# Kernel tuning notes

Hardware: AMD Instinct MI355X
Metric: run time of the kernel (lower is better)

Reference implementation:

```python
import jax, jax.numpy as jnp
import numpy as np

N_EMBD = 1024
N_HEAD = 16
HEAD_SIZE = 64


def setup_inputs() -> dict:
    key = jax.random.key(0)
    ks = jax.random.split(key, 6)
    B, T, C, H, D = 2, 2048, N_EMBD, N_HEAD, HEAD_SIZE
    s = 1.0 / np.sqrt(C)
    x = jax.random.normal(ks[0], (B, T, C), dtype=jnp.float32)
    Wq = jax.random.normal(ks[1], (H, C, D), dtype=jnp.float32) * s
    Wk = jax.random.normal(ks[2], (H, C, D), dtype=jnp.float32) * s
    Wv = jax.random.normal(ks[3], (H, C, D), dtype=jnp.float32) * s
    Wo = jax.random.normal(ks[4], (H * D, C), dtype=jnp.float32) * (1.0 / np.sqrt(H * D))
    bo = jax.random.normal(ks[5], (C,), dtype=jnp.float32) * 0.01
    return {"x": x, "Wq": Wq, "Wk": Wk, "Wv": Wv, "Wo": Wo, "bo": bo}


def reference(x, Wq, Wk, Wv, Wo, bo):
    B, T, C = x.shape
    H, _, D = Wq.shape
    # Per-head projections, batched across heads: [B,H,T,D]
    q = jnp.einsum('btc,hcd->bhtd', x, Wq)
    k = jnp.einsum('btc,hcd->bhtd', x, Wk)
    v = jnp.einsum('btc,hcd->bhtd', x, Wv)
    # NOTE: original scales by sqrt(C) = sqrt(n_embd), not sqrt(head_size)
    scale = 1.0 / jnp.sqrt(jnp.float32(C))
    att = jnp.einsum('bhtd,bhsd->bhts', q, k) * scale  # [B,H,T,T]
    causal = jnp.tril(jnp.ones((T, T), dtype=bool))
    att = jnp.where(causal, att, -jnp.inf)
    att = jax.nn.softmax(att, axis=-1)
    # dropout omitted (eval mode / deterministic reference)
    out = jnp.einsum('bhts,bhsd->bhtd', att, v)  # [B,H,T,D]
    out = out.transpose(0, 2, 1, 3).reshape(B, T, H * D)
    return out @ Wo + bo
```

## Files before the change

### kernel.cpp

```cpp
#include <hip/hip_runtime.h>
#include <hip/hip_bf16.h>


typedef __hip_bfloat16 bf16;
typedef __bf16 v8bf __attribute__((ext_vector_type(8)));
typedef float  v4f  __attribute__((ext_vector_type(4)));
typedef unsigned long long u64;
typedef unsigned int u32;

#define MFMA16(a, b, c) __builtin_amdgcn_mfma_f32_16x16x32_bf16((a), (b), (c), 0, 0, 0)

__device__ __forceinline__ bf16 f2b(float x) { return __float2bfloat16(x); }
__device__ __forceinline__ __bf16 f2braw(float x) {
  bf16 t = __float2bfloat16(x);
  return *reinterpret_cast<__bf16*>(&t);
}
__device__ __forceinline__ unsigned short f2bu(float x) {
  bf16 t = __float2bfloat16(x);
  return *reinterpret_cast<unsigned short*>(&t);
}

__device__ __forceinline__ void load16_lds(const bf16* gptr, const bf16* lptr) {
  __builtin_amdgcn_global_load_lds(
      (const __attribute__((address_space(1))) u32*)gptr,
      (__attribute__((address_space(3))) u32*)lptr, 16, 0, 0);
}

__global__ __launch_bounds__(256) void prep_kernel(
    const float* __restrict__ x,
    const float* __restrict__ Wq, const float* __restrict__ Wk,
    const float* __restrict__ Wv, const float* __restrict__ Wo,
    bf16* __restrict__ xb, bf16* __restrict__ wt, bf16* __restrict__ wot)
{
  __shared__ float Lt[32][33];
  const int bid = blockIdx.x, tid = threadIdx.x;

  if (bid < 2048) {
    size_t i = ((size_t)bid * 256 + tid) * 8;
    float4 f0 = *(const float4*)(x + i);
    float4 f1 = *(const float4*)(x + i + 4);
    v8bf v;
    v[0] = f2braw(f0.x); v[1] = f2braw(f0.y); v[2] = f2braw(f0.z); v[3] = f2braw(f0.w);
    v[4] = f2braw(f1.x); v[5] = f2braw(f1.y); v[6] = f2braw(f1.z); v[7] = f2braw(f1.w);
    *(v8bf*)(xb + i) = v;
    return;
  }
  const int tx = tid & 31, ty = tid >> 5;
  if (bid < 5120) {
    const int idx = bid - 2048;
    const int z = idx >> 6, rem = idx & 63;
    const int p = z >> 4, h = z & 15;
    const float* ib = ((p == 0) ? Wq : (p == 1) ? Wk : Wv) + (size_t)h * 65536;
    bf16* ob = wt + (size_t)z * 65536;
    const int j0 = (rem & 1) * 32, i0 = (rem >> 1) * 32;
    #pragma unroll
    for (int r = 0; r < 4; ++r)
      Lt[ty + 8 * r][tx] = ib[(size_t)(i0 + ty + 8 * r) * 64 + j0 + tx];
    __syncthreads();
    #pragma unroll
    for (int r = 0; r < 4; ++r)
      ob[(size_t)(j0 + ty + 8 * r) * 1024 + i0 + tx] = f2b(Lt[tx][ty + 8 * r]);
  } else {
    const int idx = bid - 5120;
    const int j0 = (idx & 31) * 32, i0 = (idx >> 5) * 32;
    #pragma unroll
    for (int r = 0; r < 4; ++r)
      Lt[ty + 8 * r][tx] = Wo[(size_t)(i0 + ty + 8 * r) * 1024 + j0 + tx];
    __syncthreads();
    #pragma unroll
    for (int r = 0; r < 4; ++r)
      wot[(size_t)(j0 + ty + 8 * r) * 1024 + i0 + tx] = f2b(Lt[tx][ty + 8 * r]);
  }
}

__global__ __launch_bounds__(256) void qkv_gemm_kernel(
    const bf16* __restrict__ xb, const bf16* __restrict__ wt,
    bf16* __restrict__ qkv)
{
  __shared__ __align__(16) bf16 Ash[2][128][32];
  __shared__ __align__(16) bf16 Bsh[2][128][32];

  const int mt = blockIdx.x, nt = blockIdx.y;
  const int tid = threadIdx.x, w = tid >> 6, lane = tid & 63;
  const int ln = lane & 15, quad = lane >> 4;
  const int wm = w >> 1, wn = w & 1;
  const int m0 = mt * 128, n0 = nt * 128;

  const v4f vzero = {0.f, 0.f, 0.f, 0.f};
  v4f acc[4][4];
  #pragma unroll
  for (int mf = 0; mf < 4; ++mf)
    #pragma unroll
    for (int nf = 0; nf < 4; ++nf) acc[mf][nf] = vzero;

  const int srow = lane >> 2, sseg = (lane & 3) * 8;
  const bf16* ga = xb + (size_t)(m0 + 32 * w + srow) * 1024 + sseg;
  const bf16* gb = wt + (size_t)(n0 + 32 * w + srow) * 1024 + sseg;

  {
    load16_lds(ga,             &Ash[0][32 * w][0]);
    load16_lds(ga + 16 * 1024, &Ash[0][32 * w + 16][0]);
    load16_lds(gb,             &Bsh[0][32 * w][0]);
    load16_lds(gb + 16 * 1024, &Bsh[0][32 * w + 16][0]);
  }

  for (int kt = 0; kt < 32; ++kt) {
    const int buf = kt & 1;
    __syncthreads();

    v8bf af[4], bfv[4];
    #pragma unroll
    for (int mf = 0; mf < 4; ++mf)
      af[mf] = *(const v8bf*)&Ash[buf][wm * 64 + mf * 16 + ln][quad * 8];
    #pragma unroll
    for (int nf = 0; nf < 4; ++nf)
      bfv[nf] = *(const v8bf*)&Bsh[buf][wn * 64 + nf * 16 + ln][quad * 8];

    if (kt < 31) {
      const int k0 = (kt + 1) * 32, nb = buf ^ 1;
      load16_lds(ga + k0,             &Ash[nb][32 * w][0]);
      load16_lds(ga + 16 * 1024 + k0, &Ash[nb][32 * w + 16][0]);
      load16_lds(gb + k0,             &Bsh[nb][32 * w][0]);
      load16_lds(gb + 16 * 1024 + k0, &Bsh[nb][32 * w + 16][0]);
    }

    #pragma unroll
    for (int mf = 0; mf < 4; ++mf)
      #pragma unroll
      for (int nf = 0; nf < 4; ++nf)
        acc[mf][nf] = MFMA16(af[mf], bfv[nf], acc[mf][nf]);
  }

  const int jcol0 = n0 + wn * 64;
  const int p = jcol0 >> 10;
  const int h = (jcol0 >> 6) & 15;
  const float scale = (p == 0) ? 0.03125f : 1.0f;

  if (p < 2) {
    bf16* base = qkv + (size_t)p * 4194304 + (size_t)h * 262144;
    #pragma unroll
    for (int mf = 0; mf < 4; ++mf)
      #pragma unroll
      for (int nf = 0; nf < 4; ++nf) {
        int d = nf * 16 + ln;
        #pragma unroll
        for (int r = 0; r < 4; ++r) {
          int m = m0 + wm * 64 + mf * 16 + quad * 4 + r;
          base[(size_t)m * 64 + d] = f2b(acc[mf][nf][r] * scale);
        }
      }
  } else {
    bf16* vb = qkv + (size_t)2 * 4194304 + (size_t)h * 262144;
    #pragma unroll
    for (int mf = 0; mf < 4; ++mf) {
      int mrow = m0 + wm * 64 + mf * 16 + quad * 4;
      int bi = mrow >> 11, t0 = mrow & 2047;
      #pragma unroll
      for (int nf = 0; nf < 4; ++nf) {
        int d = nf * 16 + ln;
        u64 pk = (u64)f2bu(acc[mf][nf][0]) |
                 ((u64)f2bu(acc[mf][nf][1]) << 16) |
                 ((u64)f2bu(acc[mf][nf][2]) << 32) |
                 ((u64)f2bu(acc[mf][nf][3]) << 48);
        *(u64*)(vb + (size_t)bi * 131072 + (size_t)d * 2048 + t0) = pk;
      }
    }
  }
}

__global__ __launch_bounds__(128) void attn_kernel(
    const bf16* __restrict__ qkv, bf16* __restrict__ att)
{
  __shared__ __align__(16) bf16 Ksh[2][2][64][32];
  __shared__ __align__(16) bf16 Vsh[2][2][64][32];
  __shared__ __align__(16) __bf16 Psh[2][16][72];

  const int fid = blockIdx.x;
  const int mtraw = fid & 31;
  const int mt = ((fid >> 8) & 1) ? (31 - mtraw) : mtraw;
  const int grp = (fid >> 5) & 31;
  const int b = grp >> 4, h = grp & 15;
  const int row0 = mt * 64;

  const int tid = threadIdx.x, w = tid >> 6, lane = tid & 63;
  const int ln = lane & 15, quad = lane >> 4;

  const bf16* qbase  = qkv + (size_t)h * 262144 + (size_t)b * 131072;
  const bf16* kbase  = qbase + 4194304;
  const bf16* vtbase = qbase + 8388608;

  const int wrow = row0 + w * 32;
  v8bf aq[2][2];
  #pragma unroll
  for (int mc = 0; mc < 2; ++mc)
    #pragma unroll
    for (int ks = 0; ks < 2; ++ks)
      aq[mc][ks] = *(const v8bf*)(qbase +
          (size_t)(wrow + mc * 16 + ln) * 64 + ks * 32 + quad * 8);

  v8bf vone;
  {
    unsigned short u = 0x3F80;
    __bf16 one_e = *reinterpret_cast<__bf16*>(&u);
    #pragma unroll
    for (int j = 0; j < 8; ++j) vone[j] = one_e;
  }

  const v4f vzero = {0.f, 0.f, 0.f, 0.f};
  v4f o[2][4], lacc[2];
  #pragma unroll
  for (int mc = 0; mc < 2; ++mc) {
    lacc[mc] = vzero;
    #pragma unroll
    for (int n = 0; n < 4; ++n) o[mc][n] = vzero;
  }

  const float NEG = -30000.0f;
  const int kb_end = mt;
  const int srow = lane >> 2, sseg = (lane & 3) * 8;

  const bf16* gk0 = kbase + (size_t)(w * 32 + srow) * 64 + sseg;
  const bf16* gv0 = vtbase + (size_t)(w * 32 + srow) * 2048 + sseg;

  #define STAGE(KB, BUF)                                                     \
    {                                                                        \
      const bf16* gk = gk0 + (size_t)(KB) * 64 * 64;                         \
      load16_lds(gk,            &Ksh[BUF][0][w * 32][0]);                    \
      load16_lds(gk + 32,       &Ksh[BUF][1][w * 32][0]);                    \
      load16_lds(gk + 1024,     &Ksh[BUF][0][w * 32 + 16][0]);               \
      load16_lds(gk + 1056,     &Ksh[BUF][1][w * 32 + 16][0]);               \
      const bf16* gv = gv0 + (KB) * 64;                                      \
      load16_lds(gv,            &Vsh[BUF][0][w * 32][0]);                    \
      load16_lds(gv + 32,       &Vsh[BUF][1][w * 32][0]);                    \
      load16_lds(gv + 32768,    &Vsh[BUF][0][w * 32 + 16][0]);               \
      load16_lds(gv + 32800,    &Vsh[BUF][1][w * 32 + 16][0]);               \
    }

  STAGE(0, 0)

  for (int kb = 0; kb <= kb_end; ++kb) {
    const int buf = kb & 1;
    __syncthreads();

    v8bf kf[2][4], vf[2][4];
    #pragma unroll
    for (int nf = 0; nf < 4; ++nf) {
      kf[0][nf] = *(const v8bf*)&Ksh[buf][0][nf * 16 + ln][quad * 8];
      kf[1][nf] = *(const v8bf*)&Ksh[buf][1][nf * 16 + ln][quad * 8];
      vf[0][nf] = *(const v8bf*)&Vsh[buf][0][nf * 16 + ln][quad * 8];
      vf[1][nf] = *(const v8bf*)&Vsh[buf][1][nf * 16 + ln][quad * 8];
    }

    if (kb < kb_end) STAGE(kb + 1, buf ^ 1)

    #pragma unroll
    for (int mc = 0; mc < 2; ++mc) {
      v4f s[4];
      #pragma unroll
      for (int nf = 0; nf < 4; ++nf) s[nf] = vzero;
      #pragma unroll
      for (int ks = 0; ks < 2; ++ks)
        #pragma unroll
        for (int nf = 0; nf < 4; ++nf)
          s[nf] = MFMA16(aq[mc][ks], kf[ks][nf], s[nf]);

      if (kb == kb_end) {
        int row = wrow + mc * 16 + quad * 4;
        #pragma unroll
        for (int nf = 0; nf < 4; ++nf) {
          int col = kb * 64 + nf * 16 + ln;
          #pragma unroll
          for (int r = 0; r < 4; ++r)
            if (col > row + r) s[nf][r] = NEG;
        }
      }

      #pragma unroll
      for (int nf = 0; nf < 4; ++nf)
        #pragma unroll
        for (int r = 0; r < 4; ++r)
          Psh[w][quad * 4 + r][nf * 16 + ln] = f2braw(__expf(s[nf][r]));
      __asm__ volatile("s_waitcnt lgkmcnt(0)" ::: "memory");

      #pragma unroll
      for (int ks = 0; ks < 2; ++ks) {
        v8bf pf = *(const v8bf*)&Psh[w][ln][ks * 32 + quad * 8];
        lacc[mc] = MFMA16(pf, vone, lacc[mc]);
        #pragma unroll
        for (int nf = 0; nf < 4; ++nf)
          o[mc][nf] = MFMA16(pf, vf[ks][nf], o[mc][nf]);
      }
    }
  }
  #undef STAGE

  #pragma unroll
  for (int mc = 0; mc < 2; ++mc) {
    v4f inv;
    #pragma unroll
    for (int r = 0; r < 4; ++r) inv[r] = 1.0f / lacc[mc][r];
    #pragma unroll
    for (int nf = 0; nf < 4; ++nf)
      #pragma unroll
      for (int r = 0; r < 4; ++r) {
        int m = b * 2048 + wrow + mc * 16 + quad * 4 + r;
        att[(size_t)m * 1024 + h * 64 + nf * 16 + ln] = f2b(o[mc][nf][r] * inv[r]);
      }
  }
}

__global__ __launch_bounds__(256) void out_gemm_kernel(
    const bf16* __restrict__ att, const bf16* __restrict__ wot,
    const float* __restrict__ bo, float* __restrict__ out)
{
  __shared__ __align__(16) bf16 Ash[2][128][32];
  __shared__ __align__(16) bf16 Bsh[2][64][32];

  const int mt = blockIdx.x, nt = blockIdx.y;
  const int tid = threadIdx.x, w = tid >> 6, lane = tid & 63;
  const int ln = lane & 15, quad = lane >> 4;
  const int wm = w >> 1, wn = w & 1;
  const int m0 = mt * 128, n0 = nt * 64;

  const v4f vzero = {0.f, 0.f, 0.f, 0.f};
  v4f acc[4][2];
  #pragma unroll
  for (int mf = 0; mf < 4; ++mf)
    #pragma unroll
    for (int nf = 0; nf < 2; ++nf) acc[mf][nf] = vzero;

  const int srow = lane >> 2, sseg = (lane & 3) * 8;
  const bf16* ga = att + (size_t)(m0 + 32 * w + srow) * 1024 + sseg;
  const bf16* gb = wot + (size_t)(n0 + 16 * w + srow) * 1024 + sseg;

  {
    load16_lds(ga,             &Ash[0][32 * w][0]);
    load16_lds(ga + 16 * 1024, &Ash[0][32 * w + 16][0]);
    load16_lds(gb,             &Bsh[0][16 * w][0]);
  }

  for (int kt = 0; kt < 32; ++kt) {
    const int buf = kt & 1;
    __syncthreads();

    v8bf af[4], bfv[2];
    #pragma unroll
    for (int mf = 0; mf < 4; ++mf)
      af[mf] = *(const v8bf*)&Ash[buf][wm * 64 + mf * 16 + ln][quad * 8];
    #pragma unroll
    for (int nf = 0; nf < 2; ++nf)
      bfv[nf] = *(const v8bf*)&Bsh[buf][wn * 32 + nf * 16 + ln][quad * 8];

    if (kt < 31) {
      const int k0 = (kt + 1) * 32, nb = buf ^ 1;
      load16_lds(ga + k0,             &Ash[nb][32 * w][0]);
      load16_lds(ga + 16 * 1024 + k0, &Ash[nb][32 * w + 16][0]);
      load16_lds(gb + k0,             &Bsh[nb][16 * w][0]);
    }

    #pragma unroll
    for (int mf = 0; mf < 4; ++mf)
      #pragma unroll
      for (int nf = 0; nf < 2; ++nf)
        acc[mf][nf] = MFMA16(af[mf], bfv[nf], acc[mf][nf]);
  }

  #pragma unroll
  for (int nf = 0; nf < 2; ++nf) {
    int j = n0 + wn * 32 + nf * 16 + ln;
    float bias = bo[j];
    #pragma unroll
    for (int mf = 0; mf < 4; ++mf)
      #pragma unroll
      for (int r = 0; r < 4; ++r) {
        int m = m0 + wm * 64 + mf * 16 + quad * 4 + r;
        out[(size_t)m * 1024 + j] = acc[mf][nf][r] + bias;
      }
  }
}

extern "C" void kernel_launch(void* const* d_in, const int* in_sizes, int n_in,
                              void* d_out, int out_size, void* d_ws, size_t ws_size,
                              hipStream_t stream) {
  const float* x  = (const float*)d_in[0];
  const float* Wq = (const float*)d_in[1];
  const float* Wk = (const float*)d_in[2];
  const float* Wv = (const float*)d_in[3];
  const float* Wo = (const float*)d_in[4];
  const float* bo = (const float*)d_in[5];
  float* out = (float*)d_out;

  bf16* xb  = (bf16*)d_ws;
  bf16* wt  = xb + 4194304;
  bf16* wot = xb + 7340032;
  bf16* qkv = xb + 8388608;
  bf16* att = xb + 20971520;

  prep_kernel<<<6144, 256, 0, stream>>>(x, Wq, Wk, Wv, Wo, xb, wt, wot);
  qkv_gemm_kernel<<<dim3(32, 24), 256, 0, stream>>>(xb, wt, qkv);
  attn_kernel<<<1024, 128, 0, stream>>>(qkv, att);
  out_gemm_kernel<<<dim3(32, 16), 256, 0, stream>>>(att, wot, bo, out);
}
```

Measured before the change: 182.2 us.

## Split attention KV range into two chunks with a separate combine kernel

Each attention query tile now runs as two blocks, each covering half of its causal key range. Partial unnormalized outputs and row sums go to workspace, and a new combine kernel sums them and normalizes. The goal is to double the attention grid and balance load across the triangular mask, at the cost of an extra kernel launch and more global traffic. Separately, the GEMM loops now issue the next tile's global-to-LDS prefetch before the LDS fragment reads. Op0 reuses the xb region, which is dead by the time attention runs. The softmax has no max-subtraction, so summing the two halves is valid.

```diff
diff --git a/kernel.cpp b/kernel.cpp
--- a/kernel.cpp
+++ b/kernel.cpp
@@ -108,14 +108,6 @@
     const int buf = kt & 1;
     __syncthreads();
 
-    v8bf af[4], bfv[4];
-    #pragma unroll
-    for (int mf = 0; mf < 4; ++mf)
-      af[mf] = *(const v8bf*)&Ash[buf][wm * 64 + mf * 16 + ln][quad * 8];
-    #pragma unroll
-    for (int nf = 0; nf < 4; ++nf)
-      bfv[nf] = *(const v8bf*)&Bsh[buf][wn * 64 + nf * 16 + ln][quad * 8];
-
     if (kt < 31) {
       const int k0 = (kt + 1) * 32, nb = buf ^ 1;
       load16_lds(ga + k0,             &Ash[nb][32 * w][0]);
@@ -123,6 +115,14 @@
       load16_lds(gb + k0,             &Bsh[nb][32 * w][0]);
       load16_lds(gb + 16 * 1024 + k0, &Bsh[nb][32 * w + 16][0]);
     }
+
+    v8bf af[4], bfv[4];
+    #pragma unroll
+    for (int mf = 0; mf < 4; ++mf)
+      af[mf] = *(const v8bf*)&Ash[buf][wm * 64 + mf * 16 + ln][quad * 8];
+    #pragma unroll
+    for (int nf = 0; nf < 4; ++nf)
+      bfv[nf] = *(const v8bf*)&Bsh[buf][wn * 64 + nf * 16 + ln][quad * 8];
 
     #pragma unroll
     for (int mf = 0; mf < 4; ++mf)
@@ -169,7 +169,8 @@
 }
 
 __global__ __launch_bounds__(128) void attn_kernel(
-    const bf16* __restrict__ qkv, bf16* __restrict__ att)
+    const bf16* __restrict__ qkv, bf16* __restrict__ Op0,
+    bf16* __restrict__ Op1, float* __restrict__ lp)
 {
   __shared__ __align__(16) bf16 Ksh[2][2][64][32];
   __shared__ __align__(16) bf16 Vsh[2][2][64][32];
@@ -177,10 +178,16 @@
 
   const int fid = blockIdx.x;
   const int mtraw = fid & 31;
-  const int mt = ((fid >> 8) & 1) ? (31 - mtraw) : mtraw;
-  const int grp = (fid >> 5) & 31;
+  const int chunk = (fid >> 5) & 1;
+  const int grp = (fid >> 6) & 31;
+  const int mt = ((fid >> 9) & 1) ? (31 - mtraw) : mtraw;
   const int b = grp >> 4, h = grp & 15;
   const int row0 = mt * 64;
+
+  const int ntile = mt + 1;
+  const int c0 = (ntile + 1) >> 1;
+  const int kb_lo = chunk ? c0 : 0;
+  const int kb_hi = chunk ? ntile : c0;
 
   const int tid = threadIdx.x, w = tid >> 6, lane = tid & 63;
   const int ln = lane & 15, quad = lane >> 4;
@@ -216,7 +223,6 @@
   }
 
   const float NEG = -30000.0f;
-  const int kb_end = mt;
   const int srow = lane >> 2, sseg = (lane & 3) * 8;
 
   const bf16* gk0 = kbase + (size_t)(w * 32 + srow) * 64 + sseg;
@@ -236,11 +242,13 @@
       load16_lds(gv + 32800,    &Vsh[BUF][1][w * 32 + 16][0]);               \
     }
 
-  STAGE(0, 0)
-
-  for (int kb = 0; kb <= kb_end; ++kb) {
-    const int buf = kb & 1;
+  if (kb_lo < kb_hi) STAGE(kb_lo, 0)
+
+  for (int kb = kb_lo; kb < kb_hi; ++kb) {
+    const int buf = (kb - kb_lo) & 1;
     __syncthreads();
+
+    if (kb + 1 < kb_hi) STAGE(kb + 1, buf ^ 1)
 
     v8bf kf[2][4], vf[2][4];
     #pragma unroll
@@ -251,8 +259,6 @@
       vf[1][nf] = *(const v8bf*)&Vsh[buf][1][nf * 16 + ln][quad * 8];
     }
 
-    if (kb < kb_end) STAGE(kb + 1, buf ^ 1)
-
     #pragma unroll
     for (int mc = 0; mc < 2; ++mc) {
       v4f s[4];
@@ -264,7 +270,7 @@
         for (int nf = 0; nf < 4; ++nf)
           s[nf] = MFMA16(aq[mc][ks], kf[ks][nf], s[nf]);
 
-      if (kb == kb_end) {
+      if (kb == mt) {
         int row = wrow + mc * 16 + quad * 4;
         #pragma unroll
         for (int nf = 0; nf < 4; ++nf) {
@@ -294,19 +300,40 @@
   }
   #undef STAGE
 
-  #pragma unroll
-  for (int mc = 0; mc < 2; ++mc) {
-    v4f inv;
-    #pragma unroll
-    for (int r = 0; r < 4; ++r) inv[r] = 1.0f / lacc[mc][r];
+  bf16* op = chunk ? Op1 : Op0;
+  #pragma unroll
+  for (int mc = 0; mc < 2; ++mc)
     #pragma unroll
     for (int nf = 0; nf < 4; ++nf)
       #pragma unroll
       for (int r = 0; r < 4; ++r) {
         int m = b * 2048 + wrow + mc * 16 + quad * 4 + r;
-        att[(size_t)m * 1024 + h * 64 + nf * 16 + ln] = f2b(o[mc][nf][r] * inv[r]);
-      }
-  }
+        op[(size_t)m * 1024 + h * 64 + nf * 16 + ln] = f2b(o[mc][nf][r]);
+      }
+  if (ln == 0) {
+    float* lpc = lp + chunk * 65536 + h * 4096 + b * 2048;
+    #pragma unroll
+    for (int mc = 0; mc < 2; ++mc)
+      *(v4f*)&lpc[wrow + mc * 16 + quad * 4] = lacc[mc];
+  }
+}
+
+__global__ __launch_bounds__(256) void combine_kernel(
+    const bf16* __restrict__ Op0, const bf16* __restrict__ Op1,
+    const float* __restrict__ lp, bf16* __restrict__ att)
+{
+  size_t base = ((size_t)blockIdx.x * 256 + threadIdx.x) * 8;
+  int m = (int)(base >> 10);
+  int h = ((int)base >> 6) & 15;
+  float l = lp[h * 4096 + m] + lp[65536 + h * 4096 + m];
+  float inv = 1.0f / l;
+  v8bf a = *(const v8bf*)(Op0 + base);
+  v8bf c = *(const v8bf*)(Op1 + base);
+  v8bf r;
+  #pragma unroll
+  for (int j = 0; j < 8; ++j)
+    r[j] = f2braw(((float)a[j] + (float)c[j]) * inv);
+  *(v8bf*)(att + base) = r;
 }
 
 __global__ __launch_bounds__(256) void out_gemm_kernel(
@@ -343,20 +370,20 @@
     const int buf = kt & 1;
     __syncthreads();
 
-    v8bf af[4], bfv[2];
-    #pragma unroll
-    for (int mf = 0; mf < 4; ++mf)
-      af[mf] = *(const v8bf*)&Ash[buf][wm * 64 + mf * 16 + ln][quad * 8];
-    #pragma unroll
-    for (int nf = 0; nf < 2; ++nf)
-      bfv[nf] = *(const v8bf*)&Bsh[buf][wn * 32 + nf * 16 + ln][quad * 8];
-
     if (kt < 31) {
       const int k0 = (kt + 1) * 32, nb = buf ^ 1;
       load16_lds(ga + k0,             &Ash[nb][32 * w][0]);
       load16_lds(ga + 16 * 1024 + k0, &Ash[nb][32 * w + 16][0]);
       load16_lds(gb + k0,             &Bsh[nb][16 * w][0]);
     }
+
+    v8bf af[4], bfv[2];
+    #pragma unroll
+    for (int mf = 0; mf < 4; ++mf)
+      af[mf] = *(const v8bf*)&Ash[buf][wm * 64 + mf * 16 + ln][quad * 8];
+    #pragma unroll
+    for (int nf = 0; nf < 2; ++nf)
+      bfv[nf] = *(const v8bf*)&Bsh[buf][wn * 32 + nf * 16 + ln][quad * 8];
 
     #pragma unroll
     for (int mf = 0; mf < 4; ++mf)
@@ -395,9 +422,13 @@
   bf16* wot = xb + 7340032;
   bf16* qkv = xb + 8388608;
   bf16* att = xb + 20971520;
+  bf16* Op0 = xb;
+  bf16* Op1 = xb + 25165824;
+  float* lp = (float*)(xb + 29360128);
 
   prep_kernel<<<6144, 256, 0, stream>>>(x, Wq, Wk, Wv, Wo, xb, wt, wot);
   qkv_gemm_kernel<<<dim3(32, 24), 256, 0, stream>>>(xb, wt, qkv);
-  attn_kernel<<<1024, 128, 0, stream>>>(qkv, att);
+  attn_kernel<<<2048, 128, 0, stream>>>(qkv, Op0, Op1, lp);
+  combine_kernel<<<2048, 256, 0, stream>>>(Op0, Op1, lp, att);
   out_gemm_kernel<<<dim3(32, 16), 256, 0, stream>>>(att, wot, bo, out);
 }
```

Result: slower. 208.2 us (+14.3%).

## Compute transposed scores so P stays in registers; store V as fp16

Applied to the files above, without the earlier changes.

The attention kernel now computes S^T (K as the A operand, Q as B), so each lane's exp'd probabilities already form the B operand of an fp16 16x16x16 MFMA against V^T. This removes the P round-trip through LDS, its waitcnt, and the ones-vector MFMA used for row sums. Row sums are instead accumulated in registers and reduced with shuffles. V is now written and staged as fp16 in a new LDS layout, and in the GEMMs the prefetch is issued before the LDS fragment reads. The trade-off is more MFMA instructions (K=16 instead of 32), fp16 range for P and V, and changed LDS access patterns.

```diff
diff --git a/kernel.cpp b/kernel.cpp
--- a/kernel.cpp
+++ b/kernel.cpp
@@ -5,10 +5,12 @@
 typedef __hip_bfloat16 bf16;
 typedef __bf16 v8bf __attribute__((ext_vector_type(8)));
 typedef float  v4f  __attribute__((ext_vector_type(4)));
+typedef _Float16 v4h __attribute__((ext_vector_type(4)));
 typedef unsigned long long u64;
 typedef unsigned int u32;
 
 #define MFMA16(a, b, c) __builtin_amdgcn_mfma_f32_16x16x32_bf16((a), (b), (c), 0, 0, 0)
+#define MFMAH(a, b, c)  __builtin_amdgcn_mfma_f32_16x16x16f16((a), (b), (c), 0, 0, 0)
 
 __device__ __forceinline__ bf16 f2b(float x) { return __float2bfloat16(x); }
 __device__ __forceinline__ __bf16 f2braw(float x) {
@@ -19,8 +21,12 @@
   bf16 t = __float2bfloat16(x);
   return *reinterpret_cast<unsigned short*>(&t);
 }
-
-__device__ __forceinline__ void load16_lds(const bf16* gptr, const bf16* lptr) {
+__device__ __forceinline__ unsigned short f2hu(float x) {
+  _Float16 t = (_Float16)x;
+  return *reinterpret_cast<unsigned short*>(&t);
+}
+
+__device__ __forceinline__ void load16_lds(const void* gptr, const void* lptr) {
   __builtin_amdgcn_global_load_lds(
       (const __attribute__((address_space(1))) u32*)gptr,
       (__attribute__((address_space(3))) u32*)lptr, 16, 0, 0);
@@ -108,14 +114,6 @@
     const int buf = kt & 1;
     __syncthreads();
 
-    v8bf af[4], bfv[4];
-    #pragma unroll
-    for (int mf = 0; mf < 4; ++mf)
-      af[mf] = *(const v8bf*)&Ash[buf][wm * 64 + mf * 16 + ln][quad * 8];
-    #pragma unroll
-    for (int nf = 0; nf < 4; ++nf)
-      bfv[nf] = *(const v8bf*)&Bsh[buf][wn * 64 + nf * 16 + ln][quad * 8];
-
     if (kt < 31) {
       const int k0 = (kt + 1) * 32, nb = buf ^ 1;
       load16_lds(ga + k0,             &Ash[nb][32 * w][0]);
@@ -123,6 +121,14 @@
       load16_lds(gb + k0,             &Bsh[nb][32 * w][0]);
       load16_lds(gb + 16 * 1024 + k0, &Bsh[nb][32 * w + 16][0]);
     }
+
+    v8bf af[4], bfv[4];
+    #pragma unroll
+    for (int mf = 0; mf < 4; ++mf)
+      af[mf] = *(const v8bf*)&Ash[buf][wm * 64 + mf * 16 + ln][quad * 8];
+    #pragma unroll
+    for (int nf = 0; nf < 4; ++nf)
+      bfv[nf] = *(const v8bf*)&Bsh[buf][wn * 64 + nf * 16 + ln][quad * 8];
 
     #pragma unroll
     for (int mf = 0; mf < 4; ++mf)
@@ -150,7 +156,7 @@
         }
       }
   } else {
-    bf16* vb = qkv + (size_t)2 * 4194304 + (size_t)h * 262144;
+    _Float16* vb = (_Float16*)(qkv + (size_t)2 * 4194304 + (size_t)h * 262144);
     #pragma unroll
     for (int mf = 0; mf < 4; ++mf) {
       int mrow = m0 + wm * 64 + mf * 16 + quad * 4;
@@ -158,10 +164,10 @@
       #pragma unroll
       for (int nf = 0; nf < 4; ++nf) {
         int d = nf * 16 + ln;
-        u64 pk = (u64)f2bu(acc[mf][nf][0]) |
-                 ((u64)f2bu(acc[mf][nf][1]) << 16) |
-                 ((u64)f2bu(acc[mf][nf][2]) << 32) |
-                 ((u64)f2bu(acc[mf][nf][3]) << 48);
+        u64 pk = (u64)f2hu(acc[mf][nf][0]) |
+                 ((u64)f2hu(acc[mf][nf][1]) << 16) |
+                 ((u64)f2hu(acc[mf][nf][2]) << 32) |
+                 ((u64)f2hu(acc[mf][nf][3]) << 48);
         *(u64*)(vb + (size_t)bi * 131072 + (size_t)d * 2048 + t0) = pk;
       }
     }
@@ -171,9 +177,8 @@
 __global__ __launch_bounds__(128) void attn_kernel(
     const bf16* __restrict__ qkv, bf16* __restrict__ att)
 {
-  __shared__ __align__(16) bf16 Ksh[2][2][64][32];
-  __shared__ __align__(16) bf16 Vsh[2][2][64][32];
-  __shared__ __align__(16) __bf16 Psh[2][16][72];
+  __shared__ __align__(16) bf16     Ksh[2][2][64][32];
+  __shared__ __align__(16) _Float16 Vsh[2][4][64][16];
 
   const int fid = blockIdx.x;
   const int mtraw = fid & 31;
@@ -185,9 +190,9 @@
   const int tid = threadIdx.x, w = tid >> 6, lane = tid & 63;
   const int ln = lane & 15, quad = lane >> 4;
 
-  const bf16* qbase  = qkv + (size_t)h * 262144 + (size_t)b * 131072;
-  const bf16* kbase  = qbase + 4194304;
-  const bf16* vtbase = qbase + 8388608;
+  const bf16* qbase = qkv + (size_t)h * 262144 + (size_t)b * 131072;
+  const bf16* kbase = qbase + 4194304;
+  const _Float16* vth = (const _Float16*)(qbase + 8388608);
 
   const int wrow = row0 + w * 32;
   v8bf aq[2][2];
@@ -198,42 +203,32 @@
       aq[mc][ks] = *(const v8bf*)(qbase +
           (size_t)(wrow + mc * 16 + ln) * 64 + ks * 32 + quad * 8);
 
-  v8bf vone;
-  {
-    unsigned short u = 0x3F80;
-    __bf16 one_e = *reinterpret_cast<__bf16*>(&u);
-    #pragma unroll
-    for (int j = 0; j < 8; ++j) vone[j] = one_e;
-  }
-
   const v4f vzero = {0.f, 0.f, 0.f, 0.f};
-  v4f o[2][4], lacc[2];
-  #pragma unroll
-  for (int mc = 0; mc < 2; ++mc) {
-    lacc[mc] = vzero;
-    #pragma unroll
-    for (int n = 0; n < 4; ++n) o[mc][n] = vzero;
-  }
-
-  const float NEG = -30000.0f;
+  v4f o[2][4];
+  #pragma unroll
+  for (int mc = 0; mc < 2; ++mc)
+    #pragma unroll
+    for (int dt = 0; dt < 4; ++dt) o[mc][dt] = vzero;
+  float lsum[2] = {0.f, 0.f};
+
   const int kb_end = mt;
   const int srow = lane >> 2, sseg = (lane & 3) * 8;
 
   const bf16* gk0 = kbase + (size_t)(w * 32 + srow) * 64 + sseg;
-  const bf16* gv0 = vtbase + (size_t)(w * 32 + srow) * 2048 + sseg;
+  const _Float16* gv0 = vth + (size_t)(w * 32 + (lane >> 1)) * 2048 + (lane & 1) * 8;
 
   #define STAGE(KB, BUF)                                                     \
     {                                                                        \
       const bf16* gk = gk0 + (size_t)(KB) * 64 * 64;                         \
-      load16_lds(gk,            &Ksh[BUF][0][w * 32][0]);                    \
-      load16_lds(gk + 32,       &Ksh[BUF][1][w * 32][0]);                    \
-      load16_lds(gk + 1024,     &Ksh[BUF][0][w * 32 + 16][0]);               \
-      load16_lds(gk + 1056,     &Ksh[BUF][1][w * 32 + 16][0]);               \
-      const bf16* gv = gv0 + (KB) * 64;                                      \
-      load16_lds(gv,            &Vsh[BUF][0][w * 32][0]);                    \
-      load16_lds(gv + 32,       &Vsh[BUF][1][w * 32][0]);                    \
-      load16_lds(gv + 32768,    &Vsh[BUF][0][w * 32 + 16][0]);               \
-      load16_lds(gv + 32800,    &Vsh[BUF][1][w * 32 + 16][0]);               \
+      load16_lds(gk,        &Ksh[BUF][0][w * 32][0]);                        \
+      load16_lds(gk + 32,   &Ksh[BUF][1][w * 32][0]);                        \
+      load16_lds(gk + 1024, &Ksh[BUF][0][w * 32 + 16][0]);                   \
+      load16_lds(gk + 1056, &Ksh[BUF][1][w * 32 + 16][0]);                   \
+      const _Float16* gv = gv0 + (KB) * 64;                                  \
+      load16_lds(gv,      &Vsh[BUF][0][w * 32][0]);                          \
+      load16_lds(gv + 16, &Vsh[BUF][1][w * 32][0]);                          \
+      load16_lds(gv + 32, &Vsh[BUF][2][w * 32][0]);                          \
+      load16_lds(gv + 48, &Vsh[BUF][3][w * 32][0]);                          \
     }
 
   STAGE(0, 0)
@@ -242,70 +237,68 @@
     const int buf = kb & 1;
     __syncthreads();
 
-    v8bf kf[2][4], vf[2][4];
-    #pragma unroll
-    for (int nf = 0; nf < 4; ++nf) {
-      kf[0][nf] = *(const v8bf*)&Ksh[buf][0][nf * 16 + ln][quad * 8];
-      kf[1][nf] = *(const v8bf*)&Ksh[buf][1][nf * 16 + ln][quad * 8];
-      vf[0][nf] = *(const v8bf*)&Vsh[buf][0][nf * 16 + ln][quad * 8];
-      vf[1][nf] = *(const v8bf*)&Vsh[buf][1][nf * 16 + ln][quad * 8];
-    }
-
     if (kb < kb_end) STAGE(kb + 1, buf ^ 1)
 
+    v8bf kf[2][4];
+    v4h  vf[4][4];
+    #pragma unroll
+    for (int tt = 0; tt < 4; ++tt) {
+      kf[0][tt] = *(const v8bf*)&Ksh[buf][0][tt * 16 + ln][quad * 8];
+      kf[1][tt] = *(const v8bf*)&Ksh[buf][1][tt * 16 + ln][quad * 8];
+      #pragma unroll
+      for (int dt = 0; dt < 4; ++dt)
+        vf[tt][dt] = *(const v4h*)&Vsh[buf][tt][dt * 16 + ln][quad * 4];
+    }
+
+    const bool diag = (kb == kb_end);
     #pragma unroll
     for (int mc = 0; mc < 2; ++mc) {
-      v4f s[4];
-      #pragma unroll
-      for (int nf = 0; nf < 4; ++nf) s[nf] = vzero;
+      v4f st[4];
+      #pragma unroll
+      for (int tt = 0; tt < 4; ++tt) st[tt] = vzero;
       #pragma unroll
       for (int ks = 0; ks < 2; ++ks)
         #pragma unroll
-        for (int nf = 0; nf < 4; ++nf)
-          s[nf] = MFMA16(aq[mc][ks], kf[ks][nf], s[nf]);
-
-      if (kb == kb_end) {
-        int row = wrow + mc * 16 + quad * 4;
+        for (int tt = 0; tt < 4; ++tt)
+          st[tt] = MFMA16(kf[ks][tt], aq[mc][ks], st[tt]);
+
+      const int q = wrow + mc * 16 + ln;
+      v4h p[4];
+      #pragma unroll
+      for (int tt = 0; tt < 4; ++tt) {
         #pragma unroll
-        for (int nf = 0; nf < 4; ++nf) {
-          int col = kb * 64 + nf * 16 + ln;
-          #pragma unroll
-          for (int r = 0; r < 4; ++r)
-            if (col > row + r) s[nf][r] = NEG;
+        for (int r = 0; r < 4; ++r) {
+          int t = kb * 64 + tt * 16 + quad * 4 + r;
+          float e = (diag && t > q) ? 0.f : __expf(st[tt][r]);
+          lsum[mc] += e;
+          p[tt][r] = (_Float16)e;
         }
       }
 
       #pragma unroll
-      for (int nf = 0; nf < 4; ++nf)
+      for (int dt = 0; dt < 4; ++dt)
         #pragma unroll
-        for (int r = 0; r < 4; ++r)
-          Psh[w][quad * 4 + r][nf * 16 + ln] = f2braw(__expf(s[nf][r]));
-      __asm__ volatile("s_waitcnt lgkmcnt(0)" ::: "memory");
-
-      #pragma unroll
-      for (int ks = 0; ks < 2; ++ks) {
-        v8bf pf = *(const v8bf*)&Psh[w][ln][ks * 32 + quad * 8];
-        lacc[mc] = MFMA16(pf, vone, lacc[mc]);
-        #pragma unroll
-        for (int nf = 0; nf < 4; ++nf)
-          o[mc][nf] = MFMA16(pf, vf[ks][nf], o[mc][nf]);
-      }
+        for (int tt = 0; tt < 4; ++tt)
+          o[mc][dt] = MFMAH(vf[tt][dt], p[tt], o[mc][dt]);
     }
   }
   #undef STAGE
 
   #pragma unroll
   for (int mc = 0; mc < 2; ++mc) {
-    v4f inv;
-    #pragma unroll
-    for (int r = 0; r < 4; ++r) inv[r] = 1.0f / lacc[mc][r];
-    #pragma unroll
-    for (int nf = 0; nf < 4; ++nf)
-      #pragma unroll
-      for (int r = 0; r < 4; ++r) {
-        int m = b * 2048 + wrow + mc * 16 + quad * 4 + r;
-        att[(size_t)m * 1024 + h * 64 + nf * 16 + ln] = f2b(o[mc][nf][r] * inv[r]);
-      }
+    float l = lsum[mc];
+    l += __shfl_xor(l, 16);
+    l += __shfl_xor(l, 32);
+    float inv = 1.0f / l;
+    const int m = b * 2048 + wrow + mc * 16 + ln;
+    #pragma unroll
+    for (int dt = 0; dt < 4; ++dt) {
+      u64 pk = (u64)f2bu(o[mc][dt][0] * inv) |
+               ((u64)f2bu(o[mc][dt][1] * inv) << 16) |
+               ((u64)f2bu(o[mc][dt][2] * inv) << 32) |
+               ((u64)f2bu(o[mc][dt][3] * inv) << 48);
+      *(u64*)(att + (size_t)m * 1024 + h * 64 + dt * 16 + quad * 4) = pk;
+    }
   }
 }
 
@@ -343,20 +336,20 @@
     const int buf = kt & 1;
     __syncthreads();
 
-    v8bf af[4], bfv[2];
-    #pragma unroll
-    for (int mf = 0; mf < 4; ++mf)
-      af[mf] = *(const v8bf*)&Ash[buf][wm * 64 + mf * 16 + ln][quad * 8];
-    #pragma unroll
-    for (int nf = 0; nf < 2; ++nf)
-      bfv[nf] = *(const v8bf*)&Bsh[buf][wn * 32 + nf * 16 + ln][quad * 8];
-
     if (kt < 31) {
       const int k0 = (kt + 1) * 32, nb = buf ^ 1;
       load16_lds(ga + k0,             &Ash[nb][32 * w][0]);
       load16_lds(ga + 16 * 1024 + k0, &Ash[nb][32 * w + 16][0]);
       load16_lds(gb + k0,             &Bsh[nb][16 * w][0]);
     }
+
+    v8bf af[4], bfv[2];
+    #pragma unroll
+    for (int mf = 0; mf < 4; ++mf)
+      af[mf] = *(const v8bf*)&Ash[buf][wm * 64 + mf * 16 + ln][quad * 8];
+    #pragma unroll
+    for (int nf = 0; nf < 2; ++nf)
+      bfv[nf] = *(const v8bf*)&Bsh[buf][wn * 32 + nf * 16 + ln][quad * 8];
 
     #pragma unroll
     for (int mf = 0; mf < 4; ++mf)
```

New measurement: 194.6 us. +6.8%, slower.

## Widen attention blocks to 128 query rows with paired causal tiles

Applied to the files above, without the earlier changes.

The attention kernel now runs 256 blocks of 4 waves instead of 1024 blocks of 2 waves. Each block processes two 128-row query tiles, s and 15-s, to balance causal work, and each staged K/V tile is shared by 128 query rows instead of 64. On the last K block, waves whose rows end earlier skip the compute. Separately, both GEMM kernels now issue the next async LDS prefetch before reading the current buffer into registers. The cost is fewer resident blocks per CU and sequential handling of the two tiles, which may hurt latency hiding.

```diff
diff --git a/kernel.cpp b/kernel.cpp
--- a/kernel.cpp
+++ b/kernel.cpp
@@ -20,7 +20,7 @@
   return *reinterpret_cast<unsigned short*>(&t);
 }
 
-__device__ __forceinline__ void load16_lds(const bf16* gptr, const bf16* lptr) {
+__device__ __forceinline__ void load16_lds(const void* gptr, const void* lptr) {
   __builtin_amdgcn_global_load_lds(
       (const __attribute__((address_space(1))) u32*)gptr,
       (__attribute__((address_space(3))) u32*)lptr, 16, 0, 0);
@@ -108,14 +108,6 @@
     const int buf = kt & 1;
     __syncthreads();
 
-    v8bf af[4], bfv[4];
-    #pragma unroll
-    for (int mf = 0; mf < 4; ++mf)
-      af[mf] = *(const v8bf*)&Ash[buf][wm * 64 + mf * 16 + ln][quad * 8];
-    #pragma unroll
-    for (int nf = 0; nf < 4; ++nf)
-      bfv[nf] = *(const v8bf*)&Bsh[buf][wn * 64 + nf * 16 + ln][quad * 8];
-
     if (kt < 31) {
       const int k0 = (kt + 1) * 32, nb = buf ^ 1;
       load16_lds(ga + k0,             &Ash[nb][32 * w][0]);
@@ -123,6 +115,14 @@
       load16_lds(gb + k0,             &Bsh[nb][32 * w][0]);
       load16_lds(gb + 16 * 1024 + k0, &Bsh[nb][32 * w + 16][0]);
     }
+
+    v8bf af[4], bfv[4];
+    #pragma unroll
+    for (int mf = 0; mf < 4; ++mf)
+      af[mf] = *(const v8bf*)&Ash[buf][wm * 64 + mf * 16 + ln][quad * 8];
+    #pragma unroll
+    for (int nf = 0; nf < 4; ++nf)
+      bfv[nf] = *(const v8bf*)&Bsh[buf][wn * 64 + nf * 16 + ln][quad * 8];
 
     #pragma unroll
     for (int mf = 0; mf < 4; ++mf)
@@ -168,19 +168,17 @@
   }
 }
 
-__global__ __launch_bounds__(128) void attn_kernel(
+__global__ __launch_bounds__(256) void attn_kernel(
     const bf16* __restrict__ qkv, bf16* __restrict__ att)
 {
   __shared__ __align__(16) bf16 Ksh[2][2][64][32];
   __shared__ __align__(16) bf16 Vsh[2][2][64][32];
-  __shared__ __align__(16) __bf16 Psh[2][16][72];
+  __shared__ __align__(16) __bf16 Psh[4][16][72];
 
   const int fid = blockIdx.x;
-  const int mtraw = fid & 31;
-  const int mt = ((fid >> 8) & 1) ? (31 - mtraw) : mtraw;
-  const int grp = (fid >> 5) & 31;
+  const int pair = fid & 7;
+  const int grp = fid >> 3;
   const int b = grp >> 4, h = grp & 15;
-  const int row0 = mt * 64;
 
   const int tid = threadIdx.x, w = tid >> 6, lane = tid & 63;
   const int ln = lane & 15, quad = lane >> 4;
@@ -188,15 +186,6 @@
   const bf16* qbase  = qkv + (size_t)h * 262144 + (size_t)b * 131072;
   const bf16* kbase  = qbase + 4194304;
   const bf16* vtbase = qbase + 8388608;
-
-  const int wrow = row0 + w * 32;
-  v8bf aq[2][2];
-  #pragma unroll
-  for (int mc = 0; mc < 2; ++mc)
-    #pragma unroll
-    for (int ks = 0; ks < 2; ++ks)
-      aq[mc][ks] = *(const v8bf*)(qbase +
-          (size_t)(wrow + mc * 16 + ln) * 64 + ks * 32 + quad * 8);
 
   v8bf vone;
   {
@@ -206,107 +195,119 @@
     for (int j = 0; j < 8; ++j) vone[j] = one_e;
   }
 
+  const float NEG = -30000.0f;
   const v4f vzero = {0.f, 0.f, 0.f, 0.f};
-  v4f o[2][4], lacc[2];
-  #pragma unroll
-  for (int mc = 0; mc < 2; ++mc) {
-    lacc[mc] = vzero;
-    #pragma unroll
-    for (int n = 0; n < 4; ++n) o[mc][n] = vzero;
-  }
-
-  const float NEG = -30000.0f;
-  const int kb_end = mt;
   const int srow = lane >> 2, sseg = (lane & 3) * 8;
-
-  const bf16* gk0 = kbase + (size_t)(w * 32 + srow) * 64 + sseg;
-  const bf16* gv0 = vtbase + (size_t)(w * 32 + srow) * 2048 + sseg;
+  const bf16* gk0 = kbase + (size_t)(w * 16 + srow) * 64 + sseg;
+  const bf16* gv0 = vtbase + (size_t)(w * 16 + srow) * 2048 + sseg;
 
   #define STAGE(KB, BUF)                                                     \
     {                                                                        \
-      const bf16* gk = gk0 + (size_t)(KB) * 64 * 64;                         \
-      load16_lds(gk,            &Ksh[BUF][0][w * 32][0]);                    \
-      load16_lds(gk + 32,       &Ksh[BUF][1][w * 32][0]);                    \
-      load16_lds(gk + 1024,     &Ksh[BUF][0][w * 32 + 16][0]);               \
-      load16_lds(gk + 1056,     &Ksh[BUF][1][w * 32 + 16][0]);               \
+      const bf16* gk = gk0 + (size_t)(KB) * 4096;                            \
+      load16_lds(gk,      &Ksh[BUF][0][w * 16][0]);                          \
+      load16_lds(gk + 32, &Ksh[BUF][1][w * 16][0]);                          \
       const bf16* gv = gv0 + (KB) * 64;                                      \
-      load16_lds(gv,            &Vsh[BUF][0][w * 32][0]);                    \
-      load16_lds(gv + 32,       &Vsh[BUF][1][w * 32][0]);                    \
-      load16_lds(gv + 32768,    &Vsh[BUF][0][w * 32 + 16][0]);               \
-      load16_lds(gv + 32800,    &Vsh[BUF][1][w * 32 + 16][0]);               \
-    }
-
-  STAGE(0, 0)
-
-  for (int kb = 0; kb <= kb_end; ++kb) {
-    const int buf = kb & 1;
-    __syncthreads();
-
-    v8bf kf[2][4], vf[2][4];
-    #pragma unroll
-    for (int nf = 0; nf < 4; ++nf) {
-      kf[0][nf] = *(const v8bf*)&Ksh[buf][0][nf * 16 + ln][quad * 8];
-      kf[1][nf] = *(const v8bf*)&Ksh[buf][1][nf * 16 + ln][quad * 8];
-      vf[0][nf] = *(const v8bf*)&Vsh[buf][0][nf * 16 + ln][quad * 8];
-      vf[1][nf] = *(const v8bf*)&Vsh[buf][1][nf * 16 + ln][quad * 8];
-    }
-
-    if (kb < kb_end) STAGE(kb + 1, buf ^ 1)
-
+      load16_lds(gv,      &Vsh[BUF][0][w * 16][0]);                          \
+      load16_lds(gv + 32, &Vsh[BUF][1][w * 16][0]);                          \
+    }
+
+  for (int sp = 0; sp < 2; ++sp) {
+    const int s = sp ? (15 - pair) : pair;
+    const int row0 = s * 128;
+    const int wrow = row0 + w * 32;
+    const int wk_last = 2 * s + (w >> 1);
+    const int blk_end = 2 * s + 1;
+
+    v8bf aq[2][2];
+    #pragma unroll
+    for (int mc = 0; mc < 2; ++mc)
+      #pragma unroll
+      for (int ks = 0; ks < 2; ++ks)
+        aq[mc][ks] = *(const v8bf*)(qbase +
+            (size_t)(wrow + mc * 16 + ln) * 64 + ks * 32 + quad * 8);
+
+    v4f o[2][4], lacc[2];
     #pragma unroll
     for (int mc = 0; mc < 2; ++mc) {
-      v4f s[4];
-      #pragma unroll
-      for (int nf = 0; nf < 4; ++nf) s[nf] = vzero;
-      #pragma unroll
-      for (int ks = 0; ks < 2; ++ks)
-        #pragma unroll
-        for (int nf = 0; nf < 4; ++nf)
-          s[nf] = MFMA16(aq[mc][ks], kf[ks][nf], s[nf]);
-
-      if (kb == kb_end) {
-        int row = wrow + mc * 16 + quad * 4;
+      lacc[mc] = vzero;
+      #pragma unroll
+      for (int n = 0; n < 4; ++n) o[mc][n] = vzero;
+    }
+
+    STAGE(0, 0)
+
+    for (int kb = 0; kb <= blk_end; ++kb) {
+      const int buf = kb & 1;
+      __syncthreads();
+
+      if (kb < blk_end) STAGE(kb + 1, buf ^ 1)
+
+      if (kb <= wk_last) {
+        v8bf kf[2][4], vf[2][4];
         #pragma unroll
         for (int nf = 0; nf < 4; ++nf) {
-          int col = kb * 64 + nf * 16 + ln;
+          kf[0][nf] = *(const v8bf*)&Ksh[buf][0][nf * 16 + ln][quad * 8];
+          kf[1][nf] = *(const v8bf*)&Ksh[buf][1][nf * 16 + ln][quad * 8];
+          vf[0][nf] = *(const v8bf*)&Vsh[buf][0][nf * 16 + ln][quad * 8];
+          vf[1][nf] = *(const v8bf*)&Vsh[buf][1][nf * 16 + ln][quad * 8];
+        }
+
+        #pragma unroll
+        for (int mc = 0; mc < 2; ++mc) {
+          v4f sc[4];
           #pragma unroll
-          for (int r = 0; r < 4; ++r)
-            if (col > row + r) s[nf][r] = NEG;
+          for (int nf = 0; nf < 4; ++nf) sc[nf] = vzero;
+          #pragma unroll
+          for (int ks = 0; ks < 2; ++ks)
+            #pragma unroll
+            for (int nf = 0; nf < 4; ++nf)
+              sc[nf] = MFMA16(aq[mc][ks], kf[ks][nf], sc[nf]);
+
+          if (kb == wk_last) {
+            int row = wrow + mc * 16 + quad * 4;
+            #pragma unroll
+            for (int nf = 0; nf < 4; ++nf) {
+              int col = kb * 64 + nf * 16 + ln;
+              #pragma unroll
+              for (int r = 0; r < 4; ++r)
+                if (col > row + r) sc[nf][r] = NEG;
+            }
+          }
+
+          #pragma unroll
+          for (int nf = 0; nf < 4; ++nf)
+            #pragma unroll
+            for (int r = 0; r < 4; ++r)
+              Psh[w][quad * 4 + r][nf * 16 + ln] = f2braw(__expf(sc[nf][r]));
+          __asm__ volatile("s_waitcnt lgkmcnt(0)" ::: "memory");
+
+          #pragma unroll
+          for (int ks = 0; ks < 2; ++ks) {
+            v8bf pf = *(const v8bf*)&Psh[w][ln][ks * 32 + quad * 8];
+            lacc[mc] = MFMA16(pf, vone, lacc[mc]);
+            #pragma unroll
+            for (int nf = 0; nf < 4; ++nf)
+              o[mc][nf] = MFMA16(pf, vf[ks][nf], o[mc][nf]);
+          }
         }
       }
-
+    }
+
+    #pragma unroll
+    for (int mc = 0; mc < 2; ++mc) {
+      v4f inv;
+      #pragma unroll
+      for (int r = 0; r < 4; ++r) inv[r] = 1.0f / lacc[mc][r];
       #pragma unroll
       for (int nf = 0; nf < 4; ++nf)
         #pragma unroll
-        for (int r = 0; r < 4; ++r)
-          Psh[w][quad * 4 + r][nf * 16 + ln] = f2braw(__expf(s[nf][r]));
-      __asm__ volatile("s_waitcnt lgkmcnt(0)" ::: "memory");
-
-      #pragma unroll
-      for (int ks = 0; ks < 2; ++ks) {
-        v8bf pf = *(const v8bf*)&Psh[w][ln][ks * 32 + quad * 8];
-        lacc[mc] = MFMA16(pf, vone, lacc[mc]);
-        #pragma unroll
-        for (int nf = 0; nf < 4; ++nf)
-          o[mc][nf] = MFMA16(pf, vf[ks][nf], o[mc][nf]);
-      }
+        for (int r = 0; r < 4; ++r) {
+          int m = b * 2048 + wrow + mc * 16 + quad * 4 + r;
+          att[(size_t)m * 1024 + h * 64 + nf * 16 + ln] = f2b(o[mc][nf][r] * inv[r]);
+        }
     }
   }
   #undef STAGE
-
-  #pragma unroll
-  for (int mc = 0; mc < 2; ++mc) {
-    v4f inv;
-    #pragma unroll
-    for (int r = 0; r < 4; ++r) inv[r] = 1.0f / lacc[mc][r];
-    #pragma unroll
-    for (int nf = 0; nf < 4; ++nf)
-      #pragma unroll
-      for (int r = 0; r < 4; ++r) {
-        int m = b * 2048 + wrow + mc * 16 + quad * 4 + r;
-        att[(size_t)m * 1024 + h * 64 + nf * 16 + ln] = f2b(o[mc][nf][r] * inv[r]);
-      }
-  }
 }
 
 __global__ __launch_bounds__(256) void out_gemm_kernel(
@@ -343,20 +344,20 @@
     const int buf = kt & 1;
     __syncthreads();
 
-    v8bf af[4], bfv[2];
-    #pragma unroll
-    for (int mf = 0; mf < 4; ++mf)
-      af[mf] = *(const v8bf*)&Ash[buf][wm * 64 + mf * 16 + ln][quad * 8];
-    #pragma unroll
-    for (int nf = 0; nf < 2; ++nf)
-      bfv[nf] = *(const v8bf*)&Bsh[buf][wn * 32 + nf * 16 + ln][quad * 8];
-
     if (kt < 31) {
       const int k0 = (kt + 1) * 32, nb = buf ^ 1;
       load16_lds(ga + k0,             &Ash[nb][32 * w][0]);
       load16_lds(ga + 16 * 1024 + k0, &Ash[nb][32 * w + 16][0]);
       load16_lds(gb + k0,             &Bsh[nb][16 * w][0]);
     }
+
+    v8bf af[4], bfv[2];
+    #pragma unroll
+    for (int mf = 0; mf < 4; ++mf)
+      af[mf] = *(const v8bf*)&Ash[buf][wm * 64 + mf * 16 + ln][quad * 8];
+    #pragma unroll
+    for (int nf = 0; nf < 2; ++nf)
+      bfv[nf] = *(const v8bf*)&Bsh[buf][wn * 32 + nf * 16 + ln][quad * 8];
 
     #pragma unroll
     for (int mf = 0; mf < 4; ++mf)
@@ -398,6 +399,6 @@
 
   prep_kernel<<<6144, 256, 0, stream>>>(x, Wq, Wk, Wv, Wo, xb, wt, wot);
   qkv_gemm_kernel<<<dim3(32, 24), 256, 0, stream>>>(xb, wt, qkv);
-  attn_kernel<<<1024, 128, 0, stream>>>(qkv, att);
+  attn_kernel<<<256, 256, 0, stream>>>(qkv, att);
   out_gemm_kernel<<<dim3(32, 16), 256, 0, stream>>>(att, wot, bo, out);
 }
```

Result: slower. 198.5 us (+9.0%).
